# Optimization experiments

Hardware: AMD Instinct MI355X
Metric: run time of the kernel (lower is better)

## Reference

```python
import jax, jax.numpy as jnp
import numpy as np

N_HEADS = 16
ROPE_BASE = 10000.0


def apply_rope(x):
    # x: (b, h, t, d); rotate interleaved pairs along last dim, positions = t axis
    b, h, t, d = x.shape
    theta = 1.0 / (ROPE_BASE ** (jnp.arange(0, d, 2, dtype=jnp.float32) / d))  # (d/2,)
    ang = jnp.arange(t, dtype=jnp.float32)[:, None] * theta[None, :]           # (t, d/2)
    cos = jnp.cos(ang)[None, None]  # (1,1,t,d/2)
    sin = jnp.sin(ang)[None, None]
    xp = x.reshape(b, h, t, d // 2, 2)
    x0, x1 = xp[..., 0], xp[..., 1]
    o0 = x0 * cos - x1 * sin
    o1 = x1 * cos + x0 * sin
    return jnp.stack([o0, o1], axis=-1).reshape(b, h, t, d)


def setup_inputs() -> dict:
    key = jax.random.key(0)
    k1, k2, k3 = jax.random.split(key, 3)
    B, T, C = 2, 2048, 1024
    x = jax.random.normal(k1, (B, T, C), dtype=jnp.float32)
    w_qkv = jax.random.normal(k2, (3 * C, C), dtype=jnp.float32) * (1.0 / np.sqrt(C))
    w_proj = jax.random.normal(k3, (C, C), dtype=jnp.float32) * (1.0 / np.sqrt(C))
    return {"x": x, "w_qkv": w_qkv, "w_proj": w_proj}


def reference(x, w_qkv, w_proj):
    B, T, C = x.shape
    H = N_HEADS
    D = C // H
    # fused QKV projection: (b,t,3C)
    qkv = x @ w_qkv.T
    qkv = qkv.reshape(B, T, 3, H, D).transpose(2, 0, 3, 1, 4)  # (3, b, h, t, d)
    q, k, v = qkv[0], qkv[1], qkv[2]
    q = apply_rope(q)
    k = apply_rope(k)
    scale = 1.0 / jnp.sqrt(jnp.float32(D))
    scores = jnp.einsum('bhqd,bhkd->bhqk', q, k) * scale  # (b,h,t,t)
    causal = jnp.tril(jnp.ones((T, T), dtype=bool))
    scores = jnp.where(causal[None, None], scores, jnp.finfo(scores.dtype).min)
    attn = jax.nn.softmax(scores, axis=-1)
    y = jnp.einsum('bhqk,bhkd->bhqd', attn, v)  # (b,h,t,d)
    y = y.transpose(0, 2, 1, 3).reshape(B, T, C)
    return y @ w_proj.T
```

## Files before the change

kernel.cpp:

```cpp
#include <hip/hip_runtime.h>
#include <math.h>

#define B_ 2
#define T_ 2048
#define C_ 1024
#define H_ 16
#define D_ 64
#define NX_ 4194304
#define NWQ_ 3145728
#define NWP_ 1048576

typedef unsigned short u16;
typedef unsigned int u32;
typedef __bf16 bf16x8 __attribute__((ext_vector_type(8)));
typedef _Float16 f16x8 __attribute__((ext_vector_type(8)));
typedef __fp16 fp16x2 __attribute__((ext_vector_type(2)));
typedef float f32x4 __attribute__((ext_vector_type(4)));
typedef u16 u16x4 __attribute__((ext_vector_type(4)));

__device__ __forceinline__ u16 f2bf(float f) {
    union { float f; u32 u; } v; v.f = f;
    u32 r = v.u + 0x7fffu + ((v.u >> 16) & 1u);
    return (u16)(r >> 16);
}

#define GLD_LDS(g, l) \
    __builtin_amdgcn_global_load_lds( \
        (const __attribute__((address_space(1))) u32*)(const void*)(g), \
        (__attribute__((address_space(3))) u32*)(void*)(l), 16, 0, 0)

__global__ __launch_bounds__(256) void cast_all(const float* __restrict__ x,
                                                const float* __restrict__ wq,
                                                const float* __restrict__ wp,
                                                u16* __restrict__ out,
                                                float* __restrict__ tab) {
    const int bid = blockIdx.x;
    if (bid >= 8192) {
        const int k = (bid - 8192) * 256 + threadIdx.x;
        #pragma unroll
        for (int e = 0; e < 2; ++e) {
            const int pidx = 2 * k + e;
            const int t = pidx >> 5, i = pidx & 31;
            const float theta = __expf(-0.2878231366f * (float)i);
            float sn, cs;
            __sincosf((float)t * theta, &sn, &cs);
            *(float2*)(tab + pidx * 2) = make_float2(cs, sn);
        }
        return;
    }
    const int i = (bid * 256 + threadIdx.x) * 4;
    const float* src;
    int off;
    if (i < NX_) { src = x; off = i; }
    else if (i < NX_ + NWQ_) { src = wq; off = i - NX_; }
    else { src = wp; off = i - NX_ - NWQ_; }
    float4 v = *(const float4*)(src + off);
    u16x4 o;
    o.x = f2bf(v.x); o.y = f2bf(v.y); o.z = f2bf(v.z); o.w = f2bf(v.w);
    *(u16x4*)(out + i) = o;
}

template <int EPI>
__global__ __launch_bounds__(256) void gemm64(const u16* __restrict__ A,
                                              const u16* __restrict__ Bm,
                                              float* __restrict__ OutF,
                                              u16* __restrict__ qb,
                                              u16* __restrict__ kb,
                                              u16* __restrict__ vt,
                                              const float* __restrict__ tab,
                                              int M, int N, int K) {
    __shared__ u16 As[128 * 64];
    __shared__ u16 Bs[128 * 64];
    const int tid = threadIdx.x;
    const int lane = tid & 63;
    const int wave = tid >> 6;
    const int wm = (wave >> 1) * 64;
    const int wn = (wave & 1) * 64;
    const int m0 = blockIdx.y * 128;
    const int n0 = blockIdx.x * 128;

    const int rl = lane >> 3;
    const int sg = ((lane & 7) ^ rl) * 8;
    const u16* gA[4]; const u16* gB[4];
    u16 *lA[4], *lB[4];
    #pragma unroll
    for (int c = 0; c < 4; ++c) {
        const int ca = wave * 4 + c;
        gA[c] = A + (size_t)(m0 + ca * 8 + rl) * K + sg;
        gB[c] = Bm + (size_t)(n0 + ca * 8 + rl) * K + sg;
        lA[c] = As + ca * 512;
        lB[c] = Bs + ca * 512;
    }

    const int col = lane & 15;
    const int quad = lane >> 4;
    int aoff[2][4], boff[2][4];
    #pragma unroll
    for (int ks = 0; ks < 2; ++ks)
        #pragma unroll
        for (int i = 0; i < 4; ++i) {
            const int m = wm + i * 16 + col;
            aoff[ks][i] = (m >> 3) * 512 + (m & 7) * 64 +
                          ((((ks << 2) | quad)) ^ (m & 7)) * 8;
            const int n = wn + i * 16 + col;
            boff[ks][i] = (n >> 3) * 512 + (n & 7) * 64 +
                          ((((ks << 2) | quad)) ^ (n & 7)) * 8;
        }

    f32x4 acc[4][4] = {};
    for (int k0 = 0; k0 < K; k0 += 64) {
        __syncthreads();
        #pragma unroll
        for (int c = 0; c < 4; ++c) {
            GLD_LDS(gA[c] + k0, lA[c]);
            GLD_LDS(gB[c] + k0, lB[c]);
        }
        __syncthreads();
        #pragma unroll
        for (int ks = 0; ks < 2; ++ks) {
            bf16x8 a[4], b[4];
            #pragma unroll
            for (int i = 0; i < 4; ++i) a[i] = *(const bf16x8*)(As + aoff[ks][i]);
            #pragma unroll
            for (int j = 0; j < 4; ++j) b[j] = *(const bf16x8*)(Bs + boff[ks][j]);
            #pragma unroll
            for (int i = 0; i < 4; ++i)
                #pragma unroll
                for (int j = 0; j < 4; ++j)
                    acc[i][j] = __builtin_amdgcn_mfma_f32_16x16x32_bf16(
                        a[i], b[j], acc[i][j], 0, 0, 0);
        }
    }

    const int rq = quad * 4;
    if (EPI == 0) {
        #pragma unroll
        for (int i = 0; i < 4; ++i)
            #pragma unroll
            for (int j = 0; j < 4; ++j)
                #pragma unroll
                for (int r = 0; r < 4; ++r)
                    OutF[(size_t)(m0 + wm + i * 16 + rq + r) * N +
                         n0 + wn + j * 16 + col] = acc[i][j][r];
    } else {
        const int sslot = m0 >> 10;
        #pragma unroll
        for (int i = 0; i < 4; ++i) {
            const int gm = m0 + wm + i * 16 + rq;
            const int hh = (gm >> 6) & 15;
            const int dbase = gm & 63;
            #pragma unroll
            for (int j = 0; j < 4; ++j) {
                const int gt = n0 + wn + j * 16 + col;
                const int bb = gt >> 11;
                const int t = gt & (T_ - 1);
                const int bh = bb * H_ + hh;
                if (sslot < 2) {
                    const float4 cs4 = *(const float4*)(tab + t * 64 + dbase);
                    u16x4 ov;
                    ov[0] = f2bf(acc[i][j][0] * cs4.x - acc[i][j][1] * cs4.y);
                    ov[1] = f2bf(acc[i][j][1] * cs4.x + acc[i][j][0] * cs4.y);
                    ov[2] = f2bf(acc[i][j][2] * cs4.z - acc[i][j][3] * cs4.w);
                    ov[3] = f2bf(acc[i][j][3] * cs4.z + acc[i][j][2] * cs4.w);
                    u16* dst = (sslot == 0 ? qb : kb) +
                               ((size_t)bh * T_ + t) * D_ + dbase;
                    *(u16x4*)dst = ov;
                } else {
                    #pragma unroll
                    for (int r = 0; r < 4; ++r) {
                        union { _Float16 h; u16 u; } cv;
                        cv.h = (_Float16)acc[i][j][r];
                        vt[((size_t)bh * D_ + dbase + r) * T_ + t] = cv.u;
                    }
                }
            }
        }
    }
}

__global__ __launch_bounds__(256) void attn_mfma(const u16* __restrict__ qb,
                                                 const u16* __restrict__ kb,
                                                 const u16* __restrict__ vtg,
                                                 u16* __restrict__ y) {
    __shared__ u16 Ks[2][8 * 512];
    __shared__ u16 Vt[2][8 * 512];
    const int id = blockIdx.x;
    const int qt = (id < 512) ? (31 - (id >> 5)) : ((id - 512) >> 5);
    const int bh = id & 31;
    const int b = bh >> 4, h = bh & 15;
    const int q0 = qt * 64;
    const int tid = threadIdx.x;
    const int lane = tid & 63;
    const int wave = tid >> 6;
    const int col = lane & 15;
    const int quad = lane >> 4;

    const u16* qbase = qb + ((size_t)bh * T_ + q0 + wave * 16) * D_;
    bf16x8 qf[2];
    #pragma unroll
    for (int ks = 0; ks < 2; ++ks)
        qf[ks] = *(const bf16x8*)(qbase + col * D_ + ks * 32 + quad * 8);

    f32x4 o[4] = {};
    float lsum = 0.0f;

    const int rl = lane >> 3;
    const int sg = ((lane & 7) ^ rl) * 8;
    const u16* kg[2]; const u16* vg[2];
    int lco[2];
    #pragma unroll
    for (int e = 0; e < 2; ++e) {
        const int ca = 2 * wave + e;
        kg[e] = kb + ((size_t)bh * T_ + ca * 8 + rl) * D_ + sg;
        vg[e] = vtg + ((size_t)bh * D_ + ca * 8 + rl) * T_ + sg;
        lco[e] = ca * 512;
    }

    int koff[2][4];
    #pragma unroll
    for (int ks = 0; ks < 2; ++ks)
        #pragma unroll
        for (int n = 0; n < 4; ++n) {
            const int rr = n * 16 + col;
            koff[ks][n] = (rr >> 3) * 512 + (rr & 7) * 64 +
                          ((((ks << 2) | quad)) ^ (rr & 7)) * 8;
        }

    const int srcA = col + ((quad & 1) << 5);
    const int srcB = srcA + 16;
    const bool hi = (quad >> 1) != 0;
    const int qrow = q0 + wave * 16 + col;

    const int nchunks = qt + 1;
    #pragma unroll
    for (int e = 0; e < 2; ++e) {
        GLD_LDS(kg[e], &Ks[0][lco[e]]);
        GLD_LDS(vg[e], &Vt[0][lco[e]]);
    }

    for (int ci = 0; ci < nchunks; ++ci) {
        const int buf = ci & 1;
        const int j0 = ci * 64;
        __syncthreads();
        if (ci + 1 < nchunks) {
            const size_t j1 = (size_t)(ci + 1) * 64;
            #pragma unroll
            for (int e = 0; e < 2; ++e) {
                GLD_LDS(kg[e] + j1 * D_, &Ks[buf ^ 1][lco[e]]);
                GLD_LDS(vg[e] + j1, &Vt[buf ^ 1][lco[e]]);
            }
        }

        f32x4 s[4] = {};
        #pragma unroll
        for (int ks = 0; ks < 2; ++ks)
            #pragma unroll
            for (int n = 0; n < 4; ++n) {
                const bf16x8 kf = *(const bf16x8*)(&Ks[buf][koff[ks][n]]);
                s[n] = __builtin_amdgcn_mfma_f32_16x16x32_bf16(
                    kf, qf[ks], s[n], 0, 0, 0);
            }

        const bool diag = (ci == nchunks - 1);
        u32 pk[4][2];
        #pragma unroll
        for (int n = 0; n < 4; ++n) {
            float p[4];
            #pragma unroll
            for (int r = 0; r < 4; ++r) {
                float pv = __builtin_amdgcn_exp2f(s[n][r] * 0.1803368801f);
                if (diag && (j0 + n * 16 + quad * 4 + r > qrow)) pv = 0.0f;
                p[r] = pv;
                lsum += pv;
            }
            union { fp16x2 h; u32 u; } k0, k1;
            k0.h = __builtin_amdgcn_cvt_pkrtz(p[0], p[1]);
            k1.h = __builtin_amdgcn_cvt_pkrtz(p[2], p[3]);
            pk[n][0] = k0.u;
            pk[n][1] = k1.u;
        }

        #pragma unroll
        for (int ks = 0; ks < 2; ++ks) {
            const int nl = 2 * ks, nh = nl + 1;
            const u32 w0a = __shfl(pk[nl][0], srcA), w0b = __shfl(pk[nh][0], srcA);
            const u32 w1a = __shfl(pk[nl][1], srcA), w1b = __shfl(pk[nh][1], srcA);
            const u32 w2a = __shfl(pk[nl][0], srcB), w2b = __shfl(pk[nh][0], srcB);
            const u32 w3a = __shfl(pk[nl][1], srcB), w3b = __shfl(pk[nh][1], srcB);
            union { u32 u[4]; f16x8 v; } af;
            af.u[0] = hi ? w0b : w0a;
            af.u[1] = hi ? w1b : w1a;
            af.u[2] = hi ? w2b : w2a;
            af.u[3] = hi ? w3b : w3a;
            #pragma unroll
            for (int n = 0; n < 4; ++n) {
                const f16x8 vf = *(const f16x8*)(&Vt[buf][koff[ks][n]]);
                o[n] = __builtin_amdgcn_mfma_f32_16x16x32_f16(
                    af.v, vf, o[n], 0, 0, 0);
            }
        }
    }

    float l = lsum;
    l += __shfl_xor(l, 16);
    l += __shfl_xor(l, 32);
    const float inv = 1.0f / l;
    float invr[4];
    #pragma unroll
    for (int r = 0; r < 4; ++r)
        invr[r] = __shfl(inv, quad * 4 + r);
    #pragma unroll
    for (int r = 0; r < 4; ++r) {
        const int row = q0 + wave * 16 + quad * 4 + r;
        u16* yp = y + (size_t)(b * T_ + row) * C_ + h * D_;
        #pragma unroll
        for (int n = 0; n < 4; ++n)
            yp[n * 16 + col] = f2bf(o[n][r] * invr[r]);
    }
}

extern "C" void kernel_launch(void* const* d_in, const int* in_sizes, int n_in,
                              void* d_out, int out_size, void* d_ws, size_t ws_size,
                              hipStream_t stream) {
    const float* x      = (const float*)d_in[0];
    const float* w_qkv  = (const float*)d_in[1];
    const float* w_proj = (const float*)d_in[2];
    float* out = (float*)d_out;

    const int M = B_ * T_;
    u16* xb  = (u16*)d_ws;
    u16* wqb = xb + NX_;
    u16* wpb = wqb + NWQ_;
    u16* qb  = wpb + NWP_;
    u16* kb  = qb + NX_;
    u16* vt  = kb + NX_;
    u16* yb  = vt + NX_;
    float* tab = (float*)(yb + NX_);

    cast_all<<<8192 + 128, 256, 0, stream>>>(x, w_qkv, w_proj, xb, tab);

    gemm64<1><<<dim3(M / 128, 3 * C_ / 128), 256, 0, stream>>>(
        wqb, xb, nullptr, qb, kb, vt, tab, 3 * C_, M, C_);

    attn_mfma<<<1024, 256, 0, stream>>>(qb, kb, vt, yb);

    gemm64<0><<<dim3(C_ / 128, M / 128), 256, 0, stream>>>(
        yb, wpb, out, nullptr, nullptr, nullptr, nullptr, M, C_, C_);
}
```

Measured before the change: 178.8 us.

## Load K/V MFMA fragments directly from global memory instead of LDS staging

Removes the double-buffered LDS tiles and the per-chunk barrier in the attention kernel, so each wave reads its K and V fragments straight from global memory through the caches. The diagonal chunk is peeled out so the masking test is compiled away for the other chunks, and launch bounds now request higher occupancy. The aim is to cut shared-memory traffic and synchronisation, at the cost of four times the global/cache reads per block and no explicit prefetch to hide load latency.

Result: slower. 257.0 us (+43.7%).

```diff
diff --git a/kernel.cpp b/kernel.cpp
--- a/kernel.cpp
+++ b/kernel.cpp
@@ -178,12 +178,10 @@
     }
 }
 
-__global__ __launch_bounds__(256) void attn_mfma(const u16* __restrict__ qb,
-                                                 const u16* __restrict__ kb,
-                                                 const u16* __restrict__ vtg,
-                                                 u16* __restrict__ y) {
-    __shared__ u16 Ks[2][8 * 512];
-    __shared__ u16 Vt[2][8 * 512];
+__global__ __launch_bounds__(256, 4) void attn_mfma(const u16* __restrict__ qb,
+                                                    const u16* __restrict__ kb,
+                                                    const u16* __restrict__ vtg,
+                                                    u16* __restrict__ y) {
     const int id = blockIdx.x;
     const int qt = (id < 512) ? (31 - (id >> 5)) : ((id - 512) >> 5);
     const int bh = id & 31;
@@ -204,27 +202,8 @@
     f32x4 o[4] = {};
     float lsum = 0.0f;
 
-    const int rl = lane >> 3;
-    const int sg = ((lane & 7) ^ rl) * 8;
-    const u16* kg[2]; const u16* vg[2];
-    int lco[2];
-    #pragma unroll
-    for (int e = 0; e < 2; ++e) {
-        const int ca = 2 * wave + e;
-        kg[e] = kb + ((size_t)bh * T_ + ca * 8 + rl) * D_ + sg;
-        vg[e] = vtg + ((size_t)bh * D_ + ca * 8 + rl) * T_ + sg;
-        lco[e] = ca * 512;
-    }
-
-    int koff[2][4];
-    #pragma unroll
-    for (int ks = 0; ks < 2; ++ks)
-        #pragma unroll
-        for (int n = 0; n < 4; ++n) {
-            const int rr = n * 16 + col;
-            koff[ks][n] = (rr >> 3) * 512 + (rr & 7) * 64 +
-                          ((((ks << 2) | quad)) ^ (rr & 7)) * 8;
-        }
+    const u16* kfrag = kb + ((size_t)bh * T_ + col) * D_ + quad * 8;
+    const u16* vfrag = vtg + ((size_t)bh * D_ + col) * T_ + quad * 8;
 
     const int srcA = col + ((quad & 1) << 5);
     const int srcB = srcA + 16;
@@ -232,74 +211,79 @@
     const int qrow = q0 + wave * 16 + col;
 
     const int nchunks = qt + 1;
-    #pragma unroll
-    for (int e = 0; e < 2; ++e) {
-        GLD_LDS(kg[e], &Ks[0][lco[e]]);
-        GLD_LDS(vg[e], &Vt[0][lco[e]]);
-    }
-
-    for (int ci = 0; ci < nchunks; ++ci) {
-        const int buf = ci & 1;
-        const int j0 = ci * 64;
-        __syncthreads();
-        if (ci + 1 < nchunks) {
-            const size_t j1 = (size_t)(ci + 1) * 64;
-            #pragma unroll
-            for (int e = 0; e < 2; ++e) {
-                GLD_LDS(kg[e] + j1 * D_, &Ks[buf ^ 1][lco[e]]);
-                GLD_LDS(vg[e] + j1, &Vt[buf ^ 1][lco[e]]);
-            }
-        }
-
-        f32x4 s[4] = {};
-        #pragma unroll
-        for (int ks = 0; ks < 2; ++ks)
-            #pragma unroll
-            for (int n = 0; n < 4; ++n) {
-                const bf16x8 kf = *(const bf16x8*)(&Ks[buf][koff[ks][n]]);
-                s[n] = __builtin_amdgcn_mfma_f32_16x16x32_bf16(
-                    kf, qf[ks], s[n], 0, 0, 0);
-            }
-
-        const bool diag = (ci == nchunks - 1);
-        u32 pk[4][2];
-        #pragma unroll
-        for (int n = 0; n < 4; ++n) {
-            float p[4];
-            #pragma unroll
-            for (int r = 0; r < 4; ++r) {
-                float pv = __builtin_amdgcn_exp2f(s[n][r] * 0.1803368801f);
-                if (diag && (j0 + n * 16 + quad * 4 + r > qrow)) pv = 0.0f;
-                p[r] = pv;
-                lsum += pv;
-            }
-            union { fp16x2 h; u32 u; } k0, k1;
-            k0.h = __builtin_amdgcn_cvt_pkrtz(p[0], p[1]);
-            k1.h = __builtin_amdgcn_cvt_pkrtz(p[2], p[3]);
-            pk[n][0] = k0.u;
-            pk[n][1] = k1.u;
-        }
-
-        #pragma unroll
-        for (int ks = 0; ks < 2; ++ks) {
-            const int nl = 2 * ks, nh = nl + 1;
-            const u32 w0a = __shfl(pk[nl][0], srcA), w0b = __shfl(pk[nh][0], srcA);
-            const u32 w1a = __shfl(pk[nl][1], srcA), w1b = __shfl(pk[nh][1], srcA);
-            const u32 w2a = __shfl(pk[nl][0], srcB), w2b = __shfl(pk[nh][0], srcB);
-            const u32 w3a = __shfl(pk[nl][1], srcB), w3b = __shfl(pk[nh][1], srcB);
-            union { u32 u[4]; f16x8 v; } af;
-            af.u[0] = hi ? w0b : w0a;
-            af.u[1] = hi ? w1b : w1a;
-            af.u[2] = hi ? w2b : w2a;
-            af.u[3] = hi ? w3b : w3a;
-            #pragma unroll
-            for (int n = 0; n < 4; ++n) {
-                const f16x8 vf = *(const f16x8*)(&Vt[buf][koff[ks][n]]);
-                o[n] = __builtin_amdgcn_mfma_f32_16x16x32_f16(
-                    af.v, vf, o[n], 0, 0, 0);
-            }
-        }
-    }
+
+#define CHUNK_BODY(J0, DIAG)                                                   \
+    {                                                                          \
+        const int j0_ = (J0);                                                  \
+        bf16x8 kf[2][4];                                                       \
+        f16x8 vf[2][4];                                                        \
+        _Pragma("unroll")                                                      \
+        for (int ks = 0; ks < 2; ++ks)                                         \
+            _Pragma("unroll")                                                  \
+            for (int n = 0; n < 4; ++n)                                        \
+                kf[ks][n] = *(const bf16x8*)(kfrag +                           \
+                    (size_t)(j0_ + n * 16) * D_ + ks * 32);                    \
+        _Pragma("unroll")                                                      \
+        for (int ks = 0; ks < 2; ++ks)                                         \
+            _Pragma("unroll")                                                  \
+            for (int n = 0; n < 4; ++n)                                        \
+                vf[ks][n] = *(const f16x8*)(vfrag +                            \
+                    (size_t)(n * 16) * T_ + j0_ + ks * 32);                    \
+                                 \
+        f32x4 s[4] = {};                                                       \
+        _Pragma("unroll")                                                      \
+        for (int ks = 0; ks < 2; ++ks)                                         \
+            _Pragma("unroll")                                                  \
+            for (int n = 0; n < 4; ++n)                                        \
+                s[n] = __builtin_amdgcn_mfma_f32_16x16x32_bf16(                \
+                    kf[ks][n], qf[ks], s[n], 0, 0, 0);                         \
+              \
+        u32 pk[4][2];                                                          \
+        _Pragma("unroll")                                                      \
+        for (int n = 0; n < 4; ++n) {                                          \
+            float p[4];                                                        \
+            _Pragma("unroll")                                                  \
+            for (int r = 0; r < 4; ++r) {                                      \
+                float pv = __builtin_amdgcn_exp2f(s[n][r] * 0.1803368801f);    \
+                if (DIAG && (j0_ + n * 16 + quad * 4 + r > qrow)) pv = 0.0f;   \
+                p[r] = pv;                                                     \
+                lsum += pv;                                                    \
+            }                                                                  \
+            union { fp16x2 h; u32 u; } c0, c1;                                 \
+            c0.h = __builtin_amdgcn_cvt_pkrtz(p[0], p[1]);                     \
+            c1.h = __builtin_amdgcn_cvt_pkrtz(p[2], p[3]);                     \
+            pk[n][0] = c0.u;                                                   \
+            pk[n][1] = c1.u;                                                   \
+        }                                                                      \
+                         \
+        _Pragma("unroll")                                                      \
+        for (int ks = 0; ks < 2; ++ks) {                                       \
+            const int nl = 2 * ks, nh = nl + 1;                                \
+            const u32 w0a = __shfl(pk[nl][0], srcA);                           \
+            const u32 w0b = __shfl(pk[nh][0], srcA);                           \
+            const u32 w1a = __shfl(pk[nl][1], srcA);                           \
+            const u32 w1b = __shfl(pk[nh][1], srcA);                           \
+            const u32 w2a = __shfl(pk[nl][0], srcB);                           \
+            const u32 w2b = __shfl(pk[nh][0], srcB);                           \
+            const u32 w3a = __shfl(pk[nl][1], srcB);                           \
+            const u32 w3b = __shfl(pk[nh][1], srcB);                           \
+            union { u32 u[4]; f16x8 v; } af;                                   \
+            af.u[0] = hi ? w0b : w0a;                                          \
+            af.u[1] = hi ? w1b : w1a;                                          \
+            af.u[2] = hi ? w2b : w2a;                                          \
+            af.u[3] = hi ? w3b : w3a;                                          \
+            _Pragma("unroll")                                                  \
+            for (int n = 0; n < 4; ++n)                                        \
+                o[n] = __builtin_amdgcn_mfma_f32_16x16x32_f16(                 \
+                    af.v, vf[ks][n], o[n], 0, 0, 0);                           \
+        }                                                                      \
+    }
+
+    for (int ci = 0; ci < nchunks - 1; ++ci)
+        CHUNK_BODY(ci * 64, false)
+    CHUNK_BODY((nchunks - 1) * 64, true)
+
+#undef CHUNK_BODY
 
     float l = lsum;
     l += __shfl_xor(l, 16);
```
